# Performance work log

Measured on AMD Instinct MI355X. Metric: run time of the kernel, lower is better.

The kernel has to match this reference:

```python
import jax, jax.numpy as jnp
import numpy as np

B, H, W = 4, 64, 1024
h, w = 32, 512
K = 16
C = 64
EPS = 1e-5


def setup_inputs() -> dict:
    key = jax.random.key(0)
    ks = jax.random.split(key, 8)
    n_sampled = h * w
    xyz_proj = jax.random.normal(ks[0], (B, H, W, 3), dtype=jnp.float32)
    points_proj = jax.random.normal(ks[1], (B, H, W, C), dtype=jnp.float32)
    xyz_sampled_proj = jax.random.normal(ks[2], (B, h, w, 3), dtype=jnp.float32)
    # Precomputed neighbor selection (stand-in for fused_conv_random_k, which is
    # a non-differentiable custom CUDA op producing detached indices + mask).
    neighbor_idx = jax.random.randint(ks[3], (B, n_sampled * K), 0, H * W, dtype=jnp.int32)
    valid_mask = (jax.random.uniform(ks[4], (B, n_sampled, K, 1)) > 0.1).astype(jnp.float32)
    # 1x1 conv MLP params (torch Conv2d weight (out,in,1,1) stored here as (in,out))
    def mk(k, cin, cout):
        kw, = jax.random.split(k, 1)
        wgt = jax.random.normal(kw, (cin, cout), dtype=jnp.float32) * (1.0 / np.sqrt(cin))
        return wgt
    w0 = mk(ks[5], 3 + C, 64)
    w1 = mk(ks[6], 64, 64)
    w2 = mk(ks[7], 64, 128)
    z = lambda c: jnp.zeros((c,), jnp.float32)
    o = lambda c: jnp.ones((c,), jnp.float32)
    return dict(
        xyz_proj=xyz_proj, points_proj=points_proj, xyz_sampled_proj=xyz_sampled_proj,
        neighbor_idx=neighbor_idx, valid_mask=valid_mask,
        w0=w0, b0=z(64), g0=o(64), be0=z(64), m0=z(64), v0=o(64),
        w1=w1, b1=z(64), g1=o(64), be1=z(64), m1=z(64), v1=o(64),
        w2=w2, b2=z(128), g2=o(128), be2=z(128), m2=z(128), v2=o(128),
    )


def _conv_bn_relu(x, wgt, b, g, be, m, v):
    # 1x1 conv == matmul over channel dim; BN in eval mode with running stats.
    y = jnp.einsum('bnkc,co->bnko', x, wgt) + b
    y = g * (y - m) * jax.lax.rsqrt(v + EPS) + be
    return jax.nn.relu(y)


def reference(xyz_proj, points_proj, xyz_sampled_proj, neighbor_idx, valid_mask,
              w0, b0, g0, be0, m0, v0,
              w1, b1, g1, be1, m1, v1,
              w2, b2, g2, be2, m2, v2):
    Bc = xyz_proj.shape[0]
    Cc = points_proj.shape[3]
    hh, ww = xyz_sampled_proj.shape[1], xyz_sampled_proj.shape[2]
    n_sampled = hh * ww
    xyz_bn3 = xyz_proj.reshape(Bc, -1, 3)          # (B, H*W, 3)
    points_bnc = points_proj.reshape(Bc, -1, Cc)   # (B, H*W, C)
    idx = neighbor_idx[..., None]                  # (B, n*K, 1)
    new_xyz_group = jnp.take_along_axis(xyz_bn3, idx, axis=1).reshape(Bc, n_sampled, K, 3)
    new_points_group = jnp.take_along_axis(points_bnc, idx, axis=1).reshape(Bc, n_sampled, K, Cc)
    new_xyz_group = new_xyz_group * valid_mask
    new_points_group = new_points_group * valid_mask
    new_xyz = xyz_sampled_proj.reshape(Bc, n_sampled, 1, 3)
    xyz_diff = new_xyz_group - new_xyz             # broadcast over K
    feat = jnp.concatenate([xyz_diff, new_points_group], axis=-1)  # (B, n, K, 3+C)
    feat = _conv_bn_relu(feat, w0, b0, g0, be0, m0, v0)
    feat = _conv_bn_relu(feat, w1, b1, g1, be1, m1, v1)
    feat = _conv_bn_relu(feat, w2, b2, g2, be2, m2, v2)
    points_down_sample = jnp.max(feat, axis=2)     # (B, n, 128) max-pool over K
    points_down_sample_proj = points_down_sample.reshape(Bc, hh, ww, -1)
    return points_down_sample, points_down_sample_proj
```

## Files before the change

### kernel.cpp

```cpp
#include <hip/hip_runtime.h>


#define NGRP_    8192
#define OUTHALF_ 8388608
#define XS_      72
#define WS_      72
#define EPS_     1e-5f
#define GRID_    768

typedef _Float16 h8    __attribute__((ext_vector_type(8)));
typedef float    f32x4 __attribute__((ext_vector_type(4)));

__global__ __launch_bounds__(256) void cvt_pts_kernel(
    const float* __restrict__ src, _Float16* __restrict__ dst)
{
    const size_t i = ((size_t)blockIdx.x * 256 + threadIdx.x) * 8;
    f32x4 a = *(const f32x4*)(src + i);
    f32x4 b = *(const f32x4*)(src + i + 4);
    h8 o;
#pragma unroll
    for (int j = 0; j < 4; ++j) { o[j] = (_Float16)a[j]; o[4 + j] = (_Float16)b[j]; }
    *(h8*)(dst + i) = o;
}

template<bool PRE>
__global__ __launch_bounds__(256, 3) void pnsa_main(
    const float* __restrict__ xyz,
    const void*  __restrict__ ptsv,
    const float* __restrict__ xyzs,
    const int*   __restrict__ nidx,
    const float* __restrict__ vmask,
    const float* __restrict__ w0, const float* __restrict__ b0,
    const float* __restrict__ g0, const float* __restrict__ be0,
    const float* __restrict__ m0, const float* __restrict__ v0,
    const float* __restrict__ w1, const float* __restrict__ b1,
    const float* __restrict__ g1, const float* __restrict__ be1,
    const float* __restrict__ m1, const float* __restrict__ v1,
    const float* __restrict__ w2, const float* __restrict__ b2,
    const float* __restrict__ g2, const float* __restrict__ be2,
    const float* __restrict__ m2, const float* __restrict__ v2,
    float*       __restrict__ out)
{
    __shared__ __align__(16) _Float16       ldsW1[64 * WS_];
    __shared__ __align__(16) _Float16       ldsW2[128 * WS_];
    __shared__ __align__(16) float          s1sh[64], t1sh[64];
    __shared__ __align__(16) float          s2sh[128], t2sh[128];
    __shared__ __align__(16) unsigned short ldsX[4][2][16 * XS_];

    const int tid  = threadIdx.x;
    const int wave = tid >> 6;
    const int lane = tid & 63;
    const int l15  = lane & 15;
    const int quad = lane >> 4;

    unsigned short* XbA = &ldsX[wave][0][0];
    unsigned short* XbB = &ldsX[wave][1][0];

    if (tid < 64) {
        const float s = g1[tid] * rsqrtf(v1[tid] + EPS_);
        s1sh[tid] = s;
        t1sh[tid] = (b1[tid] - m1[tid]) * s + be1[tid];
    }
    if (tid < 128) {
        const float s = g2[tid] * rsqrtf(v2[tid] + EPS_);
        s2sh[tid] = s;
        t2sh[tid] = (b2[tid] - m2[tid]) * s + be2[tid];
    }
    __syncthreads();
    for (int idx = tid; idx < 64 * 64; idx += 256) {
        const int k = idx >> 6, n = idx & 63;
        ldsW1[n * WS_ + k] = (_Float16)(w1[idx] * s1sh[n]);
    }
    for (int idx = tid; idx < 64 * 128; idx += 256) {
        const int k = idx >> 7, n = idx & 127;
        ldsW2[n * WS_ + k] = (_Float16)(w2[idx] * s2sh[n]);
    }
    __syncthreads();

    h8 b0f[4][3];
#pragma unroll
    for (int nt = 0; nt < 4; ++nt) {
        const int ch = nt * 16 + l15;
        const float s = g0[ch] * rsqrtf(v0[ch] + EPS_);
        const float t0 = (b0[ch] - m0[ch]) * s + be0[ch];
#pragma unroll
        for (int kk = 0; kk < 3; ++kk) {
            h8 f;
#pragma unroll
            for (int j = 0; j < 8; ++j) {
                const int k = kk * 32 + quad * 8 + j;
                float wv = 0.f;
                if (k < 64)       wv = w0[(3 + k) * 64 + ch] * s;
                else if (k < 67)  wv = w0[(k - 64) * 64 + ch] * s;
                else if (k == 67) wv = t0;
                f[j] = (_Float16)wv;
            }
            b0f[nt][kk] = f;
        }
    }

    const int g0i = blockIdx.x;
    const int pA0 = (g0i << 3) + (wave << 1);
    int nbA = nidx[(pA0 << 4) + l15];
    int nbB = nidx[((pA0 + 1) << 4) + l15];

    for (int grp = g0i; grp < NGRP_; grp += GRID_) {
        const int pA = (grp << 3) + (wave << 1);
        const int pB = pA + 1;
        const int gn = (grp + GRID_ < NGRP_) ? grp + GRID_ : grp;
        const int pAn = (gn << 3) + (wave << 1);

        const size_t rowA = (size_t)(((pA >> 14) << 16) + nbA);
        const size_t rowB = (size_t)(((pB >> 14) << 16) + nbB);
        h8 qA0, qA1, qB0, qB1;
        if constexpr (PRE) {
            const _Float16* pwA = (const _Float16*)ptsv + (rowA << 6);
            const _Float16* pwB = (const _Float16*)ptsv + (rowB << 6);
            qA0 = *(const h8*)(pwA + quad * 8);
            qA1 = *(const h8*)(pwA + 32 + quad * 8);
            qB0 = *(const h8*)(pwB + quad * 8);
            qB1 = *(const h8*)(pwB + 32 + quad * 8);
        } else {
            const float* pwA = (const float*)ptsv + (rowA << 6);
            const float* pwB = (const float*)ptsv + (rowB << 6);
            f32x4 r0, r1, r2, r3;
            r0 = *(const f32x4*)(pwA + quad * 8);     r1 = *(const f32x4*)(pwA + quad * 8 + 4);
            r2 = *(const f32x4*)(pwA + 32 + quad * 8); r3 = *(const f32x4*)(pwA + 32 + quad * 8 + 4);
#pragma unroll
            for (int j = 0; j < 4; ++j) { qA0[j]=(_Float16)r0[j]; qA0[4+j]=(_Float16)r1[j];
                                          qA1[j]=(_Float16)r2[j]; qA1[4+j]=(_Float16)r3[j]; }
            r0 = *(const f32x4*)(pwB + quad * 8);     r1 = *(const f32x4*)(pwB + quad * 8 + 4);
            r2 = *(const f32x4*)(pwB + 32 + quad * 8); r3 = *(const f32x4*)(pwB + 32 + quad * 8 + 4);
#pragma unroll
            for (int j = 0; j < 4; ++j) { qB0[j]=(_Float16)r0[j]; qB0[4+j]=(_Float16)r1[j];
                                          qB1[j]=(_Float16)r2[j]; qB1[4+j]=(_Float16)r3[j]; }
        }
        const float mkA = vmask[(pA << 4) + l15];
        const float mkB = vmask[(pB << 4) + l15];
        const float* xgA = xyz + rowA * 3;
        const float* xgB = xyz + rowB * 3;
        const float xgA0 = xgA[0], xgA1 = xgA[1], xgA2 = xgA[2];
        const float xgB0 = xgB[0], xgB1 = xgB[1], xgB2 = xgB[2];
        const float* xsA = xyzs + (size_t)pA * 3;
        const float* xsB = xyzs + (size_t)pB * 3;
        const float xsA0 = xsA[0], xsA1 = xsA[1], xsA2 = xsA[2];
        const float xsB0 = xsB[0], xsB1 = xsB[1], xsB2 = xsB[2];

        const int nbAn = nidx[(pAn << 4) + l15];
        const int nbBn = nidx[((pAn + 1) << 4) + l15];

        if (mkA == 0.0f) { qA0 = (h8)(_Float16)0.f; qA1 = (h8)(_Float16)0.f; }
        if (mkB == 0.0f) { qB0 = (h8)(_Float16)0.f; qB1 = (h8)(_Float16)0.f; }
        h8 aA2 = (h8)(_Float16)0.f, aB2 = (h8)(_Float16)0.f;
        if (quad == 0) {
            aA2[0] = (_Float16)(xgA0 * mkA - xsA0);
            aA2[1] = (_Float16)(xgA1 * mkA - xsA1);
            aA2[2] = (_Float16)(xgA2 * mkA - xsA2);
            aA2[3] = (_Float16)1.0f;
            aB2[0] = (_Float16)(xgB0 * mkB - xsB0);
            aB2[1] = (_Float16)(xgB1 * mkB - xsB1);
            aB2[2] = (_Float16)(xgB2 * mkB - xsB2);
            aB2[3] = (_Float16)1.0f;
        }

#pragma unroll
        for (int nt = 0; nt < 4; ++nt) {
            f32x4 accA = {0.f,0.f,0.f,0.f}, accB = {0.f,0.f,0.f,0.f};
            accA = __builtin_amdgcn_mfma_f32_16x16x32_f16(qA0, b0f[nt][0], accA, 0, 0, 0);
            accA = __builtin_amdgcn_mfma_f32_16x16x32_f16(qA1, b0f[nt][1], accA, 0, 0, 0);
            accA = __builtin_amdgcn_mfma_f32_16x16x32_f16(aA2, b0f[nt][2], accA, 0, 0, 0);
            accB = __builtin_amdgcn_mfma_f32_16x16x32_f16(qB0, b0f[nt][0], accB, 0, 0, 0);
            accB = __builtin_amdgcn_mfma_f32_16x16x32_f16(qB1, b0f[nt][1], accB, 0, 0, 0);
            accB = __builtin_amdgcn_mfma_f32_16x16x32_f16(aB2, b0f[nt][2], accB, 0, 0, 0);
#pragma unroll
            for (int r = 0; r < 4; ++r) {
                const int xi = (quad * 4 + r) * XS_ + nt * 16 + l15;
                const _Float16 hA = (_Float16)fmaxf(accA[r], 0.f);
                const _Float16 hB = (_Float16)fmaxf(accB[r], 0.f);
                XbA[xi] = __builtin_bit_cast(unsigned short, hA);
                XbB[xi] = __builtin_bit_cast(unsigned short, hB);
            }
        }

        h8 xA0 = *(const h8*)(XbA + l15 * XS_ + quad * 8);
        h8 xA1 = *(const h8*)(XbA + l15 * XS_ + 32 + quad * 8);
        h8 xB0 = *(const h8*)(XbB + l15 * XS_ + quad * 8);
        h8 xB1 = *(const h8*)(XbB + l15 * XS_ + 32 + quad * 8);
#pragma unroll 2
        for (int nt = 0; nt < 4; ++nt) {
            const _Float16* wrow = ldsW1 + (nt * 16 + l15) * WS_;
            h8 wa = *(const h8*)(wrow + quad * 8);
            h8 wb = *(const h8*)(wrow + 32 + quad * 8);
            const float t1 = t1sh[nt * 16 + l15];
            f32x4 accA = {0.f,0.f,0.f,0.f}, accB = {0.f,0.f,0.f,0.f};
            accA = __builtin_amdgcn_mfma_f32_16x16x32_f16(xA0, wa, accA, 0, 0, 0);
            accA = __builtin_amdgcn_mfma_f32_16x16x32_f16(xA1, wb, accA, 0, 0, 0);
            accB = __builtin_amdgcn_mfma_f32_16x16x32_f16(xB0, wa, accB, 0, 0, 0);
            accB = __builtin_amdgcn_mfma_f32_16x16x32_f16(xB1, wb, accB, 0, 0, 0);
#pragma unroll
            for (int r = 0; r < 4; ++r) {
                const int xi = (quad * 4 + r) * XS_ + nt * 16 + l15;
                const _Float16 hA = (_Float16)fmaxf(accA[r] + t1, 0.f);
                const _Float16 hB = (_Float16)fmaxf(accB[r] + t1, 0.f);
                XbA[xi] = __builtin_bit_cast(unsigned short, hA);
                XbB[xi] = __builtin_bit_cast(unsigned short, hB);
            }
        }

        h8 yA0 = *(const h8*)(XbA + l15 * XS_ + quad * 8);
        h8 yA1 = *(const h8*)(XbA + l15 * XS_ + 32 + quad * 8);
        h8 yB0 = *(const h8*)(XbB + l15 * XS_ + quad * 8);
        h8 yB1 = *(const h8*)(XbB + l15 * XS_ + 32 + quad * 8);
        float* obA = out + ((size_t)pA << 7);
        float* obB = out + ((size_t)pB << 7);
#pragma unroll 2
        for (int nt = 0; nt < 8; ++nt) {
            const _Float16* wrow = ldsW2 + (nt * 16 + l15) * WS_;
            h8 wa = *(const h8*)(wrow + quad * 8);
            h8 wb = *(const h8*)(wrow + 32 + quad * 8);
            const float t2 = t2sh[nt * 16 + l15];
            f32x4 accA = {0.f,0.f,0.f,0.f}, accB = {0.f,0.f,0.f,0.f};
            accA = __builtin_amdgcn_mfma_f32_16x16x32_f16(yA0, wa, accA, 0, 0, 0);
            accA = __builtin_amdgcn_mfma_f32_16x16x32_f16(yA1, wb, accA, 0, 0, 0);
            accB = __builtin_amdgcn_mfma_f32_16x16x32_f16(yB0, wa, accB, 0, 0, 0);
            accB = __builtin_amdgcn_mfma_f32_16x16x32_f16(yB1, wb, accB, 0, 0, 0);
            float vA = fmaxf(fmaxf(accA[0], accA[1]), fmaxf(accA[2], accA[3])) + t2;
            float vB = fmaxf(fmaxf(accB[0], accB[1]), fmaxf(accB[2], accB[3])) + t2;
            vA = fmaxf(vA, 0.f);  vB = fmaxf(vB, 0.f);
            vA = fmaxf(vA, __shfl_xor(vA, 16, 64));
            vA = fmaxf(vA, __shfl_xor(vA, 32, 64));
            vB = fmaxf(vB, __shfl_xor(vB, 16, 64));
            vB = fmaxf(vB, __shfl_xor(vB, 32, 64));
            if (quad == 0) {
                obA[nt * 16 + l15]            = vA;
                obA[OUTHALF_ + nt * 16 + l15] = vA;
                obB[nt * 16 + l15]            = vB;
                obB[OUTHALF_ + nt * 16 + l15] = vB;
            }
        }

        nbA = nbAn; nbB = nbBn;
    }
}

extern "C" void kernel_launch(void* const* d_in, const int* in_sizes, int n_in,
                              void* d_out, int out_size, void* d_ws, size_t ws_size,
                              hipStream_t stream) {
    const float* xyz   = (const float*)d_in[0];
    const float* pts   = (const float*)d_in[1];
    const float* xyzs  = (const float*)d_in[2];
    const int*   nidx  = (const int*)d_in[3];
    const float* vmask = (const float*)d_in[4];
    const float *w0 = (const float*)d_in[5],  *b0 = (const float*)d_in[6],
                *g0 = (const float*)d_in[7],  *be0 = (const float*)d_in[8],
                *m0 = (const float*)d_in[9],  *v0 = (const float*)d_in[10];
    const float *w1 = (const float*)d_in[11], *b1 = (const float*)d_in[12],
                *g1 = (const float*)d_in[13], *be1 = (const float*)d_in[14],
                *m1 = (const float*)d_in[15], *v1 = (const float*)d_in[16];
    const float *w2 = (const float*)d_in[17], *b2 = (const float*)d_in[18],
                *g2 = (const float*)d_in[19], *be2 = (const float*)d_in[20],
                *m2 = (const float*)d_in[21], *v2 = (const float*)d_in[22];
    float* outp = (float*)d_out;

    const size_t PTS_ELEMS = 16777216ull;
    if (ws_size >= PTS_ELEMS * sizeof(_Float16)) {
        _Float16* ptsh = (_Float16*)d_ws;
        cvt_pts_kernel<<<dim3(8192), dim3(256), 0, stream>>>(pts, ptsh);
        pnsa_main<true><<<dim3(GRID_), dim3(256), 0, stream>>>(
            xyz, (const void*)ptsh, xyzs, nidx, vmask,
            w0, b0, g0, be0, m0, v0,
            w1, b1, g1, be1, m1, v1,
            w2, b2, g2, be2, m2, v2, outp);
    } else {
        pnsa_main<false><<<dim3(GRID_), dim3(256), 0, stream>>>(
            xyz, (const void*)pts, xyzs, nidx, vmask,
            w0, b0, g0, be0, m0, v0,
            w1, b1, g1, be1, m1, v1,
            w2, b2, g2, be2, m2, v2, outp);
    }
}
```

Measured before the change: 224.5 us.

## Keep inter-layer activations in registers via permlane butterflies instead of LDS round-trips

Layers 0 and 1 now compute the transposed product (weights as A operand), so each accumulator already holds one channel per row. Packed fp16 results are redistributed into the next layer's operand layout with v_permlane16/32_swap instead of being written to and reread from per-wave LDS scratch. Bias is folded into the MFMA accumulator init, and the final max reduction uses permlane swaps instead of shfl_xor. Layer-0 weights move from registers to LDS, which frees VGPRs so occupancy rises to 4 blocks and the grid grows to 1024, at the cost of extra LDS reads per tile.

```diff
diff --git a/kernel.cpp b/kernel.cpp
--- a/kernel.cpp
+++ b/kernel.cpp
@@ -3,13 +3,14 @@
 
 #define NGRP_    8192
 #define OUTHALF_ 8388608
-#define XS_      72
 #define WS_      72
+#define W0S_     96
 #define EPS_     1e-5f
-#define GRID_    768
+#define GRID_    1024
 
 typedef _Float16 h8    __attribute__((ext_vector_type(8)));
 typedef float    f32x4 __attribute__((ext_vector_type(4)));
+typedef unsigned u32x4 __attribute__((ext_vector_type(4)));
 
 __global__ __launch_bounds__(256) void cvt_pts_kernel(
     const float* __restrict__ src, _Float16* __restrict__ dst)
@@ -23,8 +24,43 @@
     *(h8*)(dst + i) = o;
 }
 
+#define PK(lo, hi) ({                                                          \
+    const _Float16 _l = (_Float16)fmaxf((lo), 0.f);                            \
+    const _Float16 _h = (_Float16)fmaxf((hi), 0.f);                            \
+    (unsigned)__builtin_bit_cast(unsigned short, _l) |                         \
+    ((unsigned)__builtin_bit_cast(unsigned short, _h) << 16); })
+
+#define SW32(x, y) asm("v_permlane32_swap_b32 %0, %1" : "+v"(x), "+v"(y))
+#define SW16(x, y) asm("v_permlane16_swap_b32 %0, %1" : "+v"(x), "+v"(y))
+
+#define BUTTERFLY(acc, x0, x1) do {                                            \
+    unsigned _a0 = PK(acc[0][0], acc[0][1]);                                   \
+    unsigned _a1 = PK(acc[1][0], acc[1][1]);                                   \
+    unsigned _a2 = PK(acc[2][0], acc[2][1]);                                   \
+    unsigned _a3 = PK(acc[3][0], acc[3][1]);                                   \
+    unsigned _b0 = PK(acc[0][2], acc[0][3]);                                   \
+    unsigned _b1 = PK(acc[1][2], acc[1][3]);                                   \
+    unsigned _b2 = PK(acc[2][2], acc[2][3]);                                   \
+    unsigned _b3 = PK(acc[3][2], acc[3][3]);                                   \
+    SW32(_a0, _a1); SW16(_a0, _a1);                 \
+    SW32(_a2, _a3); SW16(_a2, _a3);                 \
+    SW32(_b0, _b1); SW16(_b0, _b1);                 \
+    SW32(_b2, _b3); SW16(_b2, _b3);                 \
+    u32x4 _c0 = {_a0, _b0, _a1, _b1};                                          \
+    u32x4 _c1 = {_a2, _b2, _a3, _b3};                                          \
+    x0 = __builtin_bit_cast(h8, _c0);                                          \
+    x1 = __builtin_bit_cast(h8, _c1);                                          \
+} while (0)
+
+#define XMAX16(v) do { float _t = (v);                                         \
+    asm("v_permlane16_swap_b32 %0, %1" : "+v"(v), "+v"(_t));                   \
+    (v) = fmaxf((v), _t); } while (0)
+#define XMAX32(v) do { float _t = (v);                                         \
+    asm("v_permlane32_swap_b32 %0, %1" : "+v"(v), "+v"(_t));                   \
+    (v) = fmaxf((v), _t); } while (0)
+
 template<bool PRE>
-__global__ __launch_bounds__(256, 3) void pnsa_main(
+__global__ __launch_bounds__(256, 4) void pnsa_main(
     const float* __restrict__ xyz,
     const void*  __restrict__ ptsv,
     const float* __restrict__ xyzs,
@@ -41,11 +77,11 @@
     const float* __restrict__ m2, const float* __restrict__ v2,
     float*       __restrict__ out)
 {
-    __shared__ __align__(16) _Float16       ldsW1[64 * WS_];
-    __shared__ __align__(16) _Float16       ldsW2[128 * WS_];
-    __shared__ __align__(16) float          s1sh[64], t1sh[64];
-    __shared__ __align__(16) float          s2sh[128], t2sh[128];
-    __shared__ __align__(16) unsigned short ldsX[4][2][16 * XS_];
+    __shared__ __align__(16) _Float16 ldsW0[64 * W0S_];
+    __shared__ __align__(16) _Float16 ldsW1[64 * WS_];
+    __shared__ __align__(16) _Float16 ldsW2[128 * WS_];
+    __shared__ __align__(16) float    s1sh[64];
+    __shared__ __align__(16) float    s2sh[128];
 
     const int tid  = threadIdx.x;
     const int wave = tid >> 6;
@@ -53,20 +89,10 @@
     const int l15  = lane & 15;
     const int quad = lane >> 4;
 
-    unsigned short* XbA = &ldsX[wave][0][0];
-    unsigned short* XbB = &ldsX[wave][1][0];
-
-    if (tid < 64) {
-        const float s = g1[tid] * rsqrtf(v1[tid] + EPS_);
-        s1sh[tid] = s;
-        t1sh[tid] = (b1[tid] - m1[tid]) * s + be1[tid];
-    }
-    if (tid < 128) {
-        const float s = g2[tid] * rsqrtf(v2[tid] + EPS_);
-        s2sh[tid] = s;
-        t2sh[tid] = (b2[tid] - m2[tid]) * s + be2[tid];
-    }
+    if (tid < 64)  s1sh[tid] = g1[tid] * rsqrtf(v1[tid] + EPS_);
+    if (tid < 128) s2sh[tid] = g2[tid] * rsqrtf(v2[tid] + EPS_);
     __syncthreads();
+
     for (int idx = tid; idx < 64 * 64; idx += 256) {
         const int k = idx >> 6, n = idx & 63;
         ldsW1[n * WS_ + k] = (_Float16)(w1[idx] * s1sh[n]);
@@ -75,29 +101,30 @@
         const int k = idx >> 7, n = idx & 127;
         ldsW2[n * WS_ + k] = (_Float16)(w2[idx] * s2sh[n]);
     }
+    for (int idx = tid; idx < 64 * W0S_; idx += 256) {
+        const int n = idx / W0S_, k = idx - n * W0S_;
+        const float s = g0[n] * rsqrtf(v0[n] + EPS_);
+        float wv = 0.f;
+        if (k < 64)       wv = w0[(3 + k) * 64 + n] * s;
+        else if (k < 67)  wv = w0[(k - 64) * 64 + n] * s;
+        else if (k == 67) wv = (b0[n] - m0[n]) * s + be0[n];
+        ldsW0[n * W0S_ + k] = (_Float16)wv;
+    }
     __syncthreads();
 
-    h8 b0f[4][3];
-#pragma unroll
-    for (int nt = 0; nt < 4; ++nt) {
-        const int ch = nt * 16 + l15;
-        const float s = g0[ch] * rsqrtf(v0[ch] + EPS_);
-        const float t0 = (b0[ch] - m0[ch]) * s + be0[ch];
-#pragma unroll
-        for (int kk = 0; kk < 3; ++kk) {
-            h8 f;
-#pragma unroll
-            for (int j = 0; j < 8; ++j) {
-                const int k = kk * 32 + quad * 8 + j;
-                float wv = 0.f;
-                if (k < 64)       wv = w0[(3 + k) * 64 + ch] * s;
-                else if (k < 67)  wv = w0[(k - 64) * 64 + ch] * s;
-                else if (k == 67) wv = t0;
-                f[j] = (_Float16)wv;
-            }
-            b0f[nt][kk] = f;
-        }
-    }
+    if (tid < 64)  s1sh[tid] = (b1[tid] - m1[tid]) * s1sh[tid] + be1[tid];
+    if (tid < 128) s2sh[tid] = (b2[tid] - m2[tid]) * s2sh[tid] + be2[tid];
+    __syncthreads();
+
+    f32x4 t1v[4];
+#pragma unroll
+    for (int nt = 0; nt < 4; ++nt)
+#pragma unroll
+        for (int r = 0; r < 4; ++r)
+            t1v[nt][r] = s1sh[nt * 16 + quad * 4 + r];
+    float t2v[8];
+#pragma unroll
+    for (int nt = 0; nt < 8; ++nt) t2v[nt] = s2sh[nt * 16 + l15];
 
     const int g0i = blockIdx.x;
     const int pA0 = (g0i << 3) + (wave << 1);
@@ -124,12 +151,12 @@
             const float* pwA = (const float*)ptsv + (rowA << 6);
             const float* pwB = (const float*)ptsv + (rowB << 6);
             f32x4 r0, r1, r2, r3;
-            r0 = *(const f32x4*)(pwA + quad * 8);     r1 = *(const f32x4*)(pwA + quad * 8 + 4);
+            r0 = *(const f32x4*)(pwA + quad * 8);      r1 = *(const f32x4*)(pwA + quad * 8 + 4);
             r2 = *(const f32x4*)(pwA + 32 + quad * 8); r3 = *(const f32x4*)(pwA + 32 + quad * 8 + 4);
 #pragma unroll
             for (int j = 0; j < 4; ++j) { qA0[j]=(_Float16)r0[j]; qA0[4+j]=(_Float16)r1[j];
                                           qA1[j]=(_Float16)r2[j]; qA1[4+j]=(_Float16)r3[j]; }
-            r0 = *(const f32x4*)(pwB + quad * 8);     r1 = *(const f32x4*)(pwB + quad * 8 + 4);
+            r0 = *(const f32x4*)(pwB + quad * 8);      r1 = *(const f32x4*)(pwB + quad * 8 + 4);
             r2 = *(const f32x4*)(pwB + 32 + quad * 8); r3 = *(const f32x4*)(pwB + 32 + quad * 8 + 4);
 #pragma unroll
             for (int j = 0; j < 4; ++j) { qB0[j]=(_Float16)r0[j]; qB0[4+j]=(_Float16)r1[j];
@@ -163,74 +190,60 @@
             aB2[3] = (_Float16)1.0f;
         }
 
+        f32x4 accA[4], accB[4];
 #pragma unroll
         for (int nt = 0; nt < 4; ++nt) {
-            f32x4 accA = {0.f,0.f,0.f,0.f}, accB = {0.f,0.f,0.f,0.f};
-            accA = __builtin_amdgcn_mfma_f32_16x16x32_f16(qA0, b0f[nt][0], accA, 0, 0, 0);
-            accA = __builtin_amdgcn_mfma_f32_16x16x32_f16(qA1, b0f[nt][1], accA, 0, 0, 0);
-            accA = __builtin_amdgcn_mfma_f32_16x16x32_f16(aA2, b0f[nt][2], accA, 0, 0, 0);
-            accB = __builtin_amdgcn_mfma_f32_16x16x32_f16(qB0, b0f[nt][0], accB, 0, 0, 0);
-            accB = __builtin_amdgcn_mfma_f32_16x16x32_f16(qB1, b0f[nt][1], accB, 0, 0, 0);
-            accB = __builtin_amdgcn_mfma_f32_16x16x32_f16(aB2, b0f[nt][2], accB, 0, 0, 0);
-#pragma unroll
-            for (int r = 0; r < 4; ++r) {
-                const int xi = (quad * 4 + r) * XS_ + nt * 16 + l15;
-                const _Float16 hA = (_Float16)fmaxf(accA[r], 0.f);
-                const _Float16 hB = (_Float16)fmaxf(accB[r], 0.f);
-                XbA[xi] = __builtin_bit_cast(unsigned short, hA);
-                XbB[xi] = __builtin_bit_cast(unsigned short, hB);
-            }
-        }
-
-        h8 xA0 = *(const h8*)(XbA + l15 * XS_ + quad * 8);
-        h8 xA1 = *(const h8*)(XbA + l15 * XS_ + 32 + quad * 8);
-        h8 xB0 = *(const h8*)(XbB + l15 * XS_ + quad * 8);
-        h8 xB1 = *(const h8*)(XbB + l15 * XS_ + 32 + quad * 8);
-#pragma unroll 2
+            const _Float16* wr = ldsW0 + (nt * 16 + l15) * W0S_ + quad * 8;
+            const h8 w00 = *(const h8*)(wr);
+            const h8 w01 = *(const h8*)(wr + 32);
+            const h8 w02 = *(const h8*)(wr + 64);
+            f32x4 aA = {0.f,0.f,0.f,0.f}, aB = {0.f,0.f,0.f,0.f};
+            aA = __builtin_amdgcn_mfma_f32_16x16x32_f16(w00, qA0, aA, 0, 0, 0);
+            aA = __builtin_amdgcn_mfma_f32_16x16x32_f16(w01, qA1, aA, 0, 0, 0);
+            aA = __builtin_amdgcn_mfma_f32_16x16x32_f16(w02, aA2, aA, 0, 0, 0);
+            aB = __builtin_amdgcn_mfma_f32_16x16x32_f16(w00, qB0, aB, 0, 0, 0);
+            aB = __builtin_amdgcn_mfma_f32_16x16x32_f16(w01, qB1, aB, 0, 0, 0);
+            aB = __builtin_amdgcn_mfma_f32_16x16x32_f16(w02, aB2, aB, 0, 0, 0);
+            accA[nt] = aA; accB[nt] = aB;
+        }
+        h8 xA0, xA1, xB0, xB1;
+        BUTTERFLY(accA, xA0, xA1);
+        BUTTERFLY(accB, xB0, xB1);
+
+#pragma unroll
         for (int nt = 0; nt < 4; ++nt) {
-            const _Float16* wrow = ldsW1 + (nt * 16 + l15) * WS_;
-            h8 wa = *(const h8*)(wrow + quad * 8);
-            h8 wb = *(const h8*)(wrow + 32 + quad * 8);
-            const float t1 = t1sh[nt * 16 + l15];
-            f32x4 accA = {0.f,0.f,0.f,0.f}, accB = {0.f,0.f,0.f,0.f};
-            accA = __builtin_amdgcn_mfma_f32_16x16x32_f16(xA0, wa, accA, 0, 0, 0);
-            accA = __builtin_amdgcn_mfma_f32_16x16x32_f16(xA1, wb, accA, 0, 0, 0);
-            accB = __builtin_amdgcn_mfma_f32_16x16x32_f16(xB0, wa, accB, 0, 0, 0);
-            accB = __builtin_amdgcn_mfma_f32_16x16x32_f16(xB1, wb, accB, 0, 0, 0);
-#pragma unroll
-            for (int r = 0; r < 4; ++r) {
-                const int xi = (quad * 4 + r) * XS_ + nt * 16 + l15;
-                const _Float16 hA = (_Float16)fmaxf(accA[r] + t1, 0.f);
-                const _Float16 hB = (_Float16)fmaxf(accB[r] + t1, 0.f);
-                XbA[xi] = __builtin_bit_cast(unsigned short, hA);
-                XbB[xi] = __builtin_bit_cast(unsigned short, hB);
-            }
-        }
-
-        h8 yA0 = *(const h8*)(XbA + l15 * XS_ + quad * 8);
-        h8 yA1 = *(const h8*)(XbA + l15 * XS_ + 32 + quad * 8);
-        h8 yB0 = *(const h8*)(XbB + l15 * XS_ + quad * 8);
-        h8 yB1 = *(const h8*)(XbB + l15 * XS_ + 32 + quad * 8);
+            const _Float16* wrow = ldsW1 + (nt * 16 + l15) * WS_ + quad * 8;
+            const h8 wa = *(const h8*)(wrow);
+            const h8 wb = *(const h8*)(wrow + 32);
+            f32x4 aA = t1v[nt], aB = t1v[nt];
+            aA = __builtin_amdgcn_mfma_f32_16x16x32_f16(wa, xA0, aA, 0, 0, 0);
+            aA = __builtin_amdgcn_mfma_f32_16x16x32_f16(wb, xA1, aA, 0, 0, 0);
+            aB = __builtin_amdgcn_mfma_f32_16x16x32_f16(wa, xB0, aB, 0, 0, 0);
+            aB = __builtin_amdgcn_mfma_f32_16x16x32_f16(wb, xB1, aB, 0, 0, 0);
+            accA[nt] = aA; accB[nt] = aB;
+        }
+        h8 yA0, yA1, yB0, yB1;
+        BUTTERFLY(accA, yA0, yA1);
+        BUTTERFLY(accB, yB0, yB1);
+
         float* obA = out + ((size_t)pA << 7);
         float* obB = out + ((size_t)pB << 7);
-#pragma unroll 2
+#pragma unroll
         for (int nt = 0; nt < 8; ++nt) {
-            const _Float16* wrow = ldsW2 + (nt * 16 + l15) * WS_;
-            h8 wa = *(const h8*)(wrow + quad * 8);
-            h8 wb = *(const h8*)(wrow + 32 + quad * 8);
-            const float t2 = t2sh[nt * 16 + l15];
-            f32x4 accA = {0.f,0.f,0.f,0.f}, accB = {0.f,0.f,0.f,0.f};
-            accA = __builtin_amdgcn_mfma_f32_16x16x32_f16(yA0, wa, accA, 0, 0, 0);
-            accA = __builtin_amdgcn_mfma_f32_16x16x32_f16(yA1, wb, accA, 0, 0, 0);
-            accB = __builtin_amdgcn_mfma_f32_16x16x32_f16(yB0, wa, accB, 0, 0, 0);
-            accB = __builtin_amdgcn_mfma_f32_16x16x32_f16(yB1, wb, accB, 0, 0, 0);
-            float vA = fmaxf(fmaxf(accA[0], accA[1]), fmaxf(accA[2], accA[3])) + t2;
-            float vB = fmaxf(fmaxf(accB[0], accB[1]), fmaxf(accB[2], accB[3])) + t2;
+            const _Float16* wrow = ldsW2 + (nt * 16 + l15) * WS_ + quad * 8;
+            const h8 wa = *(const h8*)(wrow);
+            const h8 wb = *(const h8*)(wrow + 32);
+            f32x4 aA = {t2v[nt], t2v[nt], t2v[nt], t2v[nt]};
+            f32x4 aB = aA;
+            aA = __builtin_amdgcn_mfma_f32_16x16x32_f16(yA0, wa, aA, 0, 0, 0);
+            aA = __builtin_amdgcn_mfma_f32_16x16x32_f16(yA1, wb, aA, 0, 0, 0);
+            aB = __builtin_amdgcn_mfma_f32_16x16x32_f16(yB0, wa, aB, 0, 0, 0);
+            aB = __builtin_amdgcn_mfma_f32_16x16x32_f16(yB1, wb, aB, 0, 0, 0);
+            float vA = fmaxf(fmaxf(aA[0], aA[1]), fmaxf(aA[2], aA[3]));
+            float vB = fmaxf(fmaxf(aB[0], aB[1]), fmaxf(aB[2], aB[3]));
             vA = fmaxf(vA, 0.f);  vB = fmaxf(vB, 0.f);
-            vA = fmaxf(vA, __shfl_xor(vA, 16, 64));
-            vA = fmaxf(vA, __shfl_xor(vA, 32, 64));
-            vB = fmaxf(vB, __shfl_xor(vB, 16, 64));
-            vB = fmaxf(vB, __shfl_xor(vB, 32, 64));
+            XMAX16(vA); XMAX32(vA);
+            XMAX16(vB); XMAX32(vB);
             if (quad == 0) {
                 obA[nt * 16 + l15]            = vA;
                 obA[OUTHALF_ + nt * 16 + l15] = vA;
```

Result: slower. 354.4 us (+57.8%).
